# Kernel optimization log

Hardware: AMD Instinct MI355X
Metric: run time of the kernel (lower is better)

The kernel has to match this reference:

```python
import jax, jax.numpy as jnp
import numpy as np

B, P, K, KS = 512, 64, 30, 4      # graphs, nodes per graph, sort-pool k, conv1d kernel
N, E, F, H = B * P, 524288, 128, 256
N_CLASSES = 10
L_OUT = K - KS + 1                 # 27, conv1d output length


def _sage(h, wl, wr, b, src, dst, inv_deg):
    # PyG SAGEConv (mean aggr): out = lin_l(mean_j x_j) + lin_r(x_i); bias only on lin_l
    agg = jax.ops.segment_sum(h[src], dst, num_segments=N) * inv_deg
    return jax.nn.relu(agg @ wl + b + h @ wr)


def setup_inputs() -> dict:
    key = jax.random.key(0)
    ks = jax.random.split(key, 32)
    x = jax.random.normal(ks[0], (N, F), jnp.float32)
    # intra-graph random edges (src -> dst aggregation)
    g = jax.random.randint(ks[1], (E,), 0, B)
    src = g * P + jax.random.randint(ks[2], (E,), 0, P)
    dst = g * P + jax.random.randint(ks[3], (E,), 0, P)
    edge_index = jnp.stack([src, dst]).astype(jnp.int32)
    batch = jnp.repeat(jnp.arange(B), P).astype(jnp.int32)  # sorted graph ids

    def lin(k, i, o):
        return jax.random.normal(k, (i, o), jnp.float32) / np.float32(np.sqrt(i))

    inp = {"x": x, "edge_index": edge_index, "batch": batch}
    dims = [(F, H), (H, H), (H, H), (H, H)]
    ki = 4
    for li, (i, o) in enumerate(dims):
        inp[f"sage{li}_wl"] = lin(ks[ki], i, o); ki += 1
        inp[f"sage{li}_wr"] = lin(ks[ki], i, o); ki += 1
        inp[f"sage{li}_b"] = jnp.zeros((o,), jnp.float32)
    inp["conv1d_w"] = jax.random.normal(ks[ki], (H, H, KS), jnp.float32) / np.float32(np.sqrt(H * KS)); ki += 1
    inp["conv1d_b"] = jnp.zeros((H,), jnp.float32)
    inp["lin1_w"] = lin(ks[ki], H * L_OUT, H); ki += 1
    inp["lin1_b"] = jnp.zeros((H,), jnp.float32)
    inp["lin2_w"] = lin(ks[ki], H, 128); ki += 1
    inp["lin2_b"] = jnp.zeros((128,), jnp.float32)
    inp["out_w"] = lin(ks[ki], 128, N_CLASSES); ki += 1
    inp["out_b"] = jnp.zeros((N_CLASSES,), jnp.float32)
    return inp


def reference(x, edge_index, batch,
              sage0_wl, sage0_wr, sage0_b,
              sage1_wl, sage1_wr, sage1_b,
              sage2_wl, sage2_wr, sage2_b,
              sage3_wl, sage3_wr, sage3_b,
              conv1d_w, conv1d_b, lin1_w, lin1_b,
              lin2_w, lin2_b, out_w, out_b):
    src, dst = edge_index[0], edge_index[1]
    deg = jax.ops.segment_sum(jnp.ones(src.shape, x.dtype), dst, num_segments=N)
    inv_deg = (1.0 / jnp.maximum(deg, 1.0))[:, None]

    h = jnp.nan_to_num(x, nan=0.0)
    h = _sage(h, sage0_wl, sage0_wr, sage0_b, src, dst, inv_deg)
    h = _sage(h, sage1_wl, sage1_wr, sage1_b, src, dst, inv_deg)
    h = _sage(h, sage2_wl, sage2_wr, sage2_b, src, dst, inv_deg)
    h = _sage(h, sage3_wl, sage3_wr, sage3_b, src, dst, inv_deg)  # [N, H]

    # SortAggregation(k=K): to dense batch, sort by last channel desc, top-k, zero-pad
    counts = jax.ops.segment_sum(jnp.ones(N, jnp.int32), batch, num_segments=B)
    offsets = jnp.cumsum(counts) - counts
    pos = jnp.arange(N) - offsets[batch]
    D = h.shape[1]
    dense = jnp.zeros((B, P, D), h.dtype).at[batch, pos].set(h)
    valid = jnp.zeros((B, P), bool).at[batch, pos].set(True)
    skey = jnp.where(valid, dense[..., -1], -jnp.inf)
    order = jnp.argsort(-skey, axis=1)[:, :K]                       # [B, K]
    topk = jnp.take_along_axis(dense, order[..., None], axis=1)     # [B, K, D]
    tvalid = jnp.take_along_axis(valid, order, axis=1)
    topk = jnp.where(tvalid[..., None], topk, 0.0)

    # x.view(B, K, -1).permute(0, 2, 1) -> [B, D, K]
    xc = topk.transpose(0, 2, 1)
    y = jax.lax.conv_general_dilated(xc, conv1d_w, (1,), 'VALID',
                                     dimension_numbers=('NCH', 'OIH', 'NCH'))
    y = jax.nn.relu(y + conv1d_b[None, :, None])                    # [B, H, L_OUT]
    y = y.reshape(B, -1)                                            # dropout is identity in eval
    y = jax.nn.relu(y @ lin1_w + lin1_b)
    y = jax.nn.relu(y @ lin2_w + lin2_b)
    return jax.nn.relu(y @ out_w + out_b)                           # [B, N_CLASSES]
```

## Files before the change

### kernel.cpp

```cpp
#include <hip/hip_runtime.h>
#include <hip/hip_bf16.h>

#define NNODES 32768
#define NEDGES 524288
#define NGRAPH 512
#define PNODES 64
#define KTOP 30
#define FIN 128
#define HID 256
#define LOUT 27

#define C1F 4.8828125e-4f
#define C2F 2.384185791015625e-7f

using f16x8 = __attribute__((ext_vector_type(8))) _Float16;
using f16x4 = __attribute__((ext_vector_type(4))) _Float16;
using f32x4 = __attribute__((ext_vector_type(4))) float;
using f32x16 = __attribute__((ext_vector_type(16))) float;

#define GLDS(src, dst) __builtin_amdgcn_global_load_lds( \
    (const __attribute__((address_space(1))) void*)(src), \
    (__attribute__((address_space(3))) void*)(dst), 16, 0, 0)

__global__ void hist_kernel(const int* __restrict__ dst, int* __restrict__ counts) {
    int e = blockIdx.x * blockDim.x + threadIdx.x;
    if (e < NEDGES) atomicAdd(&counts[dst[e]], 1);
}

__global__ __launch_bounds__(1024) void scan_block_kernel(const int* __restrict__ counts,
        int* __restrict__ loc, int* __restrict__ partial) {
    int b = blockIdx.x, t = threadIdx.x;
    int i = b * 1024 + t;
    int v = counts[i];
    int lane = t & 63, w = t >> 6;
    int x = v;
    #pragma unroll
    for (int d = 1; d < 64; d <<= 1) { int y = __shfl_up(x, d, 64); if (lane >= d) x += y; }
    __shared__ int ws[16];
    if (lane == 63) ws[w] = x;
    __syncthreads();
    if (w == 0) {
        int s = (lane < 16) ? ws[lane] : 0;
        #pragma unroll
        for (int d = 1; d < 16; d <<= 1) { int y = __shfl_up(s, d, 64); if (lane >= d) s += y; }
        if (lane < 16) ws[lane] = s;
    }
    __syncthreads();
    int base = (w > 0) ? ws[w - 1] : 0;
    int incl = base + x;
    loc[i] = incl - v;
    if (t == 1023) partial[b] = incl;
}

__global__ __launch_bounds__(1024) void scan_fixup_kernel(const int* __restrict__ loc,
        const int* __restrict__ partial, const int* __restrict__ counts,
        int* __restrict__ offsets, int* __restrict__ cursor, float* __restrict__ invdeg) {
    int b = blockIdx.x, t = threadIdx.x;
    int i = b * 1024 + t;
    __shared__ int sbase;
    if (t == 0) { int s = 0; for (int j = 0; j < b; ++j) s += partial[j]; sbase = s; }
    __syncthreads();
    int o = loc[i] + sbase;
    offsets[i] = o;
    cursor[i] = o;
    invdeg[i] = 1.0f / fmaxf((float)counts[i], 1.0f);
}

__global__ void scatter_kernel(const int* __restrict__ src, const int* __restrict__ dst,
        int* __restrict__ cursor, int* __restrict__ ssrc) {
    int e = blockIdx.x * blockDim.x + threadIdx.x;
    if (e < NEDGES) {
        int d = dst[e];
        int p = atomicAdd(&cursor[d], 1);
        ssrc[p] = src[e];
    }
}

__global__ void nan2num_split_kernel(const float* __restrict__ x,
        _Float16* __restrict__ oh, _Float16* __restrict__ ol, int n4) {
    int i = blockIdx.x * blockDim.x + threadIdx.x;
    if (i >= n4) return;
    float4 v = *(const float4*)(x + i * 4);
    float xs[4] = {v.x, v.y, v.z, v.w};
    f16x4 hh, ll;
    #pragma unroll
    for (int q = 0; q < 4; ++q) {
        float a = xs[q];
        a = (a != a) ? 0.f : a;
        _Float16 h = (_Float16)a;
        hh[q] = h;
        ll[q] = (_Float16)((a - (float)h) * 2048.0f);
    }
    *(f16x4*)(oh + (size_t)i * 4) = hh;
    *(f16x4*)(ol + (size_t)i * 4) = ll;
}

struct Prep8 {
    const float* src[8];
    _Float16* dh[8];
    _Float16* dl[8];
    int logK[8];
    int nelem[8];
    int rstride[8];
};

__global__ __launch_bounds__(256) void prep8_kernel(Prep8 p) {
    int y = blockIdx.y;
    int idx = blockIdx.x * 256 + threadIdx.x;
    if (idx >= p.nelem[y]) return;
    int lk = p.logK[y], K = 1 << lk;
    int n = idx >> lk, k = idx & (K - 1);
    float w = p.src[y][(size_t)k * 256 + n];
    _Float16 h = (_Float16)w;
    p.dh[y][(size_t)n * p.rstride[y] + k] = h;
    p.dl[y][(size_t)n * p.rstride[y] + k] = (_Float16)((w - (float)h) * 2048.0f);
}

__global__ __launch_bounds__(256) void prep_conv_kernel(const float* __restrict__ W,
        _Float16* __restrict__ b0, _Float16* __restrict__ b1) {
    int idx = blockIdx.x * 256 + threadIdx.x;
    int o = idx >> 10, k = idx & 1023;
    float w = W[(size_t)o * 1024 + (k & 255) * 4 + (k >> 8)];
    _Float16 h = (_Float16)w;
    b0[(size_t)o * 1024 + k] = h;
    b1[(size_t)o * 1024 + k] = (_Float16)((w - (float)h) * 2048.0f);
}

__global__ __launch_bounds__(256) void prep_lin1_kernel(const float* __restrict__ l1w,
        _Float16* __restrict__ wh, _Float16* __restrict__ wl_) {
    __shared__ float sh[64][65];
    int kb = blockIdx.x * 64;
    int nb = blockIdx.y * 64;
    int t = threadIdx.x;
    {
        int kk = t >> 2;
        int nc = (t & 3) * 16;
        int k = kb + kk, l = k >> 8, c = k & 255;
        const float* srow = l1w + (size_t)(c * 27 + l) * 256 + nb + nc;
        #pragma unroll
        for (int j = 0; j < 16; j += 4) {
            float4 v = *(const float4*)(srow + j);
            sh[kk][nc + j + 0] = v.x;
            sh[kk][nc + j + 1] = v.y;
            sh[kk][nc + j + 2] = v.z;
            sh[kk][nc + j + 3] = v.w;
        }
    }
    __syncthreads();
    {
        int nn = t >> 2;
        int kc = (t & 3) * 16;
        f16x8 oh[2], ol[2];
        #pragma unroll
        for (int j = 0; j < 16; ++j) {
            float x = sh[kc + j][nn];
            _Float16 h = (_Float16)x;
            oh[j >> 3][j & 7] = h;
            ol[j >> 3][j & 7] = (_Float16)((x - (float)h) * 2048.0f);
        }
        size_t o = (size_t)(nb + nn) * 6912 + kb + kc;
        *(f16x8*)(wh + o) = oh[0];
        *(f16x8*)(wh + o + 8) = oh[1];
        *(f16x8*)(wl_ + o) = ol[0];
        *(f16x8*)(wl_ + o + 8) = ol[1];
    }
}

template<int HIN, int LOGHIN>
__global__ __launch_bounds__(512, 2) void fused_sage_kernel(
        const _Float16* __restrict__ hh, const _Float16* __restrict__ hl,
        const int* __restrict__ offsets, const int* __restrict__ counts,
        const int* __restrict__ ssrc, const float* __restrict__ invdeg,
        const _Float16* __restrict__ Wh, const _Float16* __restrict__ Wl,
        const float* __restrict__ bias,
        _Float16* __restrict__ outh, _Float16* __restrict__ outl) {
    constexpr int KV = 2 * HIN;
    constexpr int NP = HIN / 32;
    constexpr int TILE = 64 * HIN;
    __shared__ __align__(16) float hsm[TILE];
    __shared__ __align__(16) _Float16 am[2][TILE];
    _Float16* hp0 = reinterpret_cast<_Float16*>(hsm);
    _Float16* hp1 = hp0 + TILE;
    const int g = blockIdx.x, t = threadIdx.x;
    const int lane = t & 63, wave = t >> 6;
    const size_t base = (size_t)g * TILE;

    for (int i4 = t * 4; i4 < TILE; i4 += 2048) {
        f16x4 vh = *(const f16x4*)(hh + base + i4);
        f16x4 vl = *(const f16x4*)(hl + base + i4);
        int row = i4 >> LOGHIN, col = i4 & (HIN - 1);
        int sw = row & 28;
        *(float4*)&hsm[(row << LOGHIN) + (col ^ sw)] = make_float4(
            (float)vh[0] + C1F * (float)vl[0],
            (float)vh[1] + C1F * (float)vl[1],
            (float)vh[2] + C1F * (float)vl[2],
            (float)vh[3] + C1F * (float)vl[3]);
    }
    __syncthreads();

    const int node = t >> 3, q = t & 7;
    const int gnode = g * 64 + node;
    const int beg = offsets[gnode], cnt = counts[gnode];
    const float s = invdeg[gnode];
    float acc[NP][4];
    #pragma unroll
    for (int p = 0; p < NP; ++p) { acc[p][0] = 0.f; acc[p][1] = 0.f; acc[p][2] = 0.f; acc[p][3] = 0.f; }
    for (int e = 0; e < cnt; ++e) {
        int sn = ssrc[beg + e] & 63;
        int ro = sn << LOGHIN, sw = sn & 28;
        #pragma unroll
        for (int p = 0; p < NP; ++p) {
            int f = p * 32 + q * 4;
            float4 v = *(const float4*)&hsm[ro + (f ^ sw)];
            acc[p][0] += v.x; acc[p][1] += v.y; acc[p][2] += v.z; acc[p][3] += v.w;
        }
    }
    float hv[NP][4];
    {
        int ro = node << LOGHIN, sw = node & 28;
        #pragma unroll
        for (int p = 0; p < NP; ++p) {
            int f = p * 32 + q * 4;
            float4 v = *(const float4*)&hsm[ro + (f ^ sw)];
            hv[p][0] = v.x; hv[p][1] = v.y; hv[p][2] = v.z; hv[p][3] = v.w;
        }
    }
    __syncthreads();

    {
        int slot = ((q >> 1) ^ (node & 3)) * 8 + (q & 1) * 4;
        int a0 = node * 32 + slot;
        #pragma unroll
        for (int p = 0; p < NP; ++p) {
            int addr = p * 2048 + a0;
            f16x4 ah, al, bh4, bl4;
            #pragma unroll
            for (int j = 0; j < 4; ++j) {
                float va = acc[p][j] * s;
                _Float16 h1 = (_Float16)va;
                ah[j] = h1; al[j] = (_Float16)((va - (float)h1) * 2048.0f);
                float vb = hv[p][j];
                _Float16 h2 = (_Float16)vb;
                bh4[j] = h2; bl4[j] = (_Float16)((vb - (float)h2) * 2048.0f);
            }
            *(f16x4*)&am[0][addr] = ah;
            *(f16x4*)&am[1][addr] = al;
            *(f16x4*)&hp0[addr] = bh4;
            *(f16x4*)&hp1[addr] = bl4;
        }
    }
    __syncthreads();

    const int l31 = lane & 31, hb = lane >> 5;
    const int col = wave * 32 + l31;
    const _Float16* __restrict__ Brh = Wh + (size_t)col * KV;
    const _Float16* __restrict__ Brl = Wl + (size_t)col * KV;
    f32x16 acc0[2], acc1[2];
    #pragma unroll
    for (int mi = 0; mi < 2; ++mi) { acc0[mi] = 0.f; acc1[mi] = 0.f; }

    f16x8 a0f[2][2][2], a1f[2][2][2];
    f16x8 bhf[2][2], blf[2][2];
    constexpr int nC = KV / 32;

    auto loadA = [&](int c, int buf) {
        int kv = c * 32;
        const _Float16* sh = (kv < HIN) ? &am[0][0] : hp0;
        const _Float16* sl = (kv < HIN) ? &am[1][0] : hp1;
        int pbase = ((kv & (HIN - 1)) >> 5) * 2048;
        #pragma unroll
        for (int h2 = 0; h2 < 2; ++h2)
            #pragma unroll
            for (int mi = 0; mi < 2; ++mi) {
                int row = mi * 32 + l31;
                int addr = pbase + row * 32 + (((2 * h2 + hb) ^ (row & 3)) * 8);
                a0f[buf][h2][mi] = *(const f16x8*)&sh[addr];
                a1f[buf][h2][mi] = *(const f16x8*)&sl[addr];
            }
    };
    auto loadB = [&](int c, int buf) {
        int kv = c * 32;
        #pragma unroll
        for (int h2 = 0; h2 < 2; ++h2) {
            int o = kv + h2 * 16 + hb * 8;
            bhf[buf][h2] = *(const f16x8*)(Brh + o);
            blf[buf][h2] = *(const f16x8*)(Brl + o);
        }
    };

    loadA(0, 0); loadB(0, 0);
    #pragma unroll 2
    for (int c = 0; c < nC; ++c) {
        int cur = c & 1, nxt = cur ^ 1;
        if (c + 1 < nC) { loadA(c + 1, nxt); loadB(c + 1, nxt); }
        #pragma unroll
        for (int h2 = 0; h2 < 2; ++h2)
            #pragma unroll
            for (int mi = 0; mi < 2; ++mi) {
                acc0[mi] = __builtin_amdgcn_mfma_f32_32x32x16_f16(a0f[cur][h2][mi], bhf[cur][h2], acc0[mi], 0, 0, 0);
                acc1[mi] = __builtin_amdgcn_mfma_f32_32x32x16_f16(a1f[cur][h2][mi], bhf[cur][h2], acc1[mi], 0, 0, 0);
                acc1[mi] = __builtin_amdgcn_mfma_f32_32x32x16_f16(a0f[cur][h2][mi], blf[cur][h2], acc1[mi], 0, 0, 0);
            }
    }

    const int rq = 4 * hb;
    const float bb = bias[col];
    #pragma unroll
    for (int mi = 0; mi < 2; ++mi) {
        #pragma unroll
        for (int reg = 0; reg < 16; ++reg) {
            float v = acc0[mi][reg] + C1F * acc1[mi][reg];
            int row = mi * 32 + (reg & 3) + 8 * (reg >> 2) + rq;
            v = fmaxf(v + bb, 0.f);
            _Float16 h1 = (_Float16)v;
            size_t o = (size_t)(g * 64 + row) * HID + col;
            outh[o] = h1;
            outl[o] = (_Float16)((v - (float)h1) * 2048.0f);
        }
    }
}

template<int NPROD, int CONV, int NPAIRS, int EPI>
__global__ __launch_bounds__(256, 2) void mfma_ps_kernel(
        const _Float16* __restrict__ A1h, const _Float16* __restrict__ A1l,
        const _Float16* __restrict__ A2h, const _Float16* __restrict__ A2l,
        const _Float16* __restrict__ B1h, const _Float16* __restrict__ B1l,
        const _Float16* __restrict__ B2h, const _Float16* __restrict__ B2l,
        const float* __restrict__ bias,
        _Float16* __restrict__ outh, _Float16* __restrict__ outl,
        float* __restrict__ Cpart,
        int lda, int K, int Nd, int nrb) {
    __shared__ _Float16 As[2][2][128 * 32];
    __shared__ _Float16 Bs[2][2][128 * 32];
    const int t = threadIdx.x;
    const int lane = t & 63, wave = t >> 6;
    const int wr = wave & 1, wc = wave >> 1;
    const int bid = blockIdx.x;
    const int rb = bid % nrb, cb = bid / nrb;
    const int row0 = rb * 128, col0 = cb * 128;
    const int l31 = lane & 31, hb = lane >> 5, x3 = l31 & 3;
    const int r16 = lane >> 2;
    const int qsrc8 = ((lane & 3) ^ (r16 & 3)) * 8;
    size_t aoffj[2], boffj[2];
    #pragma unroll
    for (int j = 0; j < 2; ++j) {
        int ar = row0 + wave * 32 + j * 16 + r16;
        aoffj[j] = CONV ? ((size_t)ar * 256 + (size_t)(ar / 27) * 768)
                        : (size_t)ar * (size_t)lda;
        boffj[j] = (size_t)(col0 + wave * 32 + j * 16 + r16) * (size_t)K;
    }
    int aroff[2], broff[2], slot8[2];
    #pragma unroll
    for (int mi = 0; mi < 2; ++mi) aroff[mi] = (wr * 64 + mi * 32 + l31) * 32;
    #pragma unroll
    for (int ni = 0; ni < 2; ++ni) broff[ni] = (wc * 64 + ni * 32 + l31) * 32;
    #pragma unroll
    for (int h = 0; h < 2; ++h) slot8[h] = ((2 * h + hb) ^ x3) * 8;

    const int KV = NPAIRS * K;
    const int kchunk = KV / gridDim.z;
    const int kv_lo = blockIdx.z * kchunk, kv_hi = kv_lo + kchunk;

    f32x16 acc0[2][2], acc1[2][2], acc2[2][2];
    #pragma unroll
    for (int i = 0; i < 2; ++i)
        #pragma unroll
        for (int j = 0; j < 2; ++j) { acc0[i][j] = 0.f; acc1[i][j] = 0.f; acc2[i][j] = 0.f; }

    auto stage = [&](int kv, int b) {
        int p = (NPAIRS == 2 && kv >= K) ? 1 : 0;
        int k = kv - p * K;
        const _Float16* __restrict__ sAh = p ? A2h : A1h;
        const _Float16* __restrict__ sAl = p ? A2l : A1l;
        const _Float16* __restrict__ sBh = p ? B2h : B1h;
        const _Float16* __restrict__ sBl = p ? B2l : B1l;
        #pragma unroll
        for (int j = 0; j < 2; ++j) {
            int ldsbase = (wave * 32 + j * 16) * 32;
            size_t ga = aoffj[j] + k + qsrc8;
            size_t gb = boffj[j] + k + qsrc8;
            GLDS(sAh + ga, &As[b][0][ldsbase]);
            GLDS(sAl + ga, &As[b][1][ldsbase]);
            GLDS(sBh + gb, &Bs[b][0][ldsbase]);
            GLDS(sBl + gb, &Bs[b][1][ldsbase]);
        }
    };

    stage(kv_lo, 0);
    __syncthreads();
    int b = 0;
    for (int kv = kv_lo; kv < kv_hi; kv += 32) {
        if (kv + 32 < kv_hi) stage(kv + 32, b ^ 1);
        #pragma unroll
        for (int h = 0; h < 2; ++h) {
            f16x8 af0[2], af1[2], bf0[2], bf1[2];
            #pragma unroll
            for (int mi = 0; mi < 2; ++mi) {
                af0[mi] = *(const f16x8*)&As[b][0][aroff[mi] + slot8[h]];
                af1[mi] = *(const f16x8*)&As[b][1][aroff[mi] + slot8[h]];
            }
            #pragma unroll
            for (int ni = 0; ni < 2; ++ni) {
                bf0[ni] = *(const f16x8*)&Bs[b][0][broff[ni] + slot8[h]];
                bf1[ni] = *(const f16x8*)&Bs[b][1][broff[ni] + slot8[h]];
            }
            #pragma unroll
            for (int mi = 0; mi < 2; ++mi)
                #pragma unroll
                for (int ni = 0; ni < 2; ++ni) {
                    acc0[mi][ni] = __builtin_amdgcn_mfma_f32_32x32x16_f16(af0[mi], bf0[ni], acc0[mi][ni], 0, 0, 0);
                    acc1[mi][ni] = __builtin_amdgcn_mfma_f32_32x32x16_f16(af1[mi], bf0[ni], acc1[mi][ni], 0, 0, 0);
                    acc1[mi][ni] = __builtin_amdgcn_mfma_f32_32x32x16_f16(af0[mi], bf1[ni], acc1[mi][ni], 0, 0, 0);
                    if (NPROD == 4)
                        acc2[mi][ni] = __builtin_amdgcn_mfma_f32_32x32x16_f16(af1[mi], bf1[ni], acc2[mi][ni], 0, 0, 0);
                }
        }
        b ^= 1;
        __syncthreads();
    }

    const int rquad = 4 * hb;
    #pragma unroll
    for (int ni = 0; ni < 2; ++ni) {
        int col = col0 + wc * 64 + ni * 32 + l31;
        float bb = (EPI == 0) ? bias[col] : 0.f;
        #pragma unroll
        for (int mi = 0; mi < 2; ++mi) {
            #pragma unroll
            for (int reg = 0; reg < 16; ++reg) {
                float v = acc0[mi][ni][reg] + C1F * acc1[mi][ni][reg];
                if (NPROD == 4) v += C2F * acc2[mi][ni][reg];
                int row = row0 + wr * 64 + mi * 32 + (reg & 3) + 8 * (reg >> 2) + rquad;
                if (EPI == 0) {
                    v = fmaxf(v + bb, 0.f);
                    _Float16 h = (_Float16)v;
                    size_t o = (size_t)row * Nd + col;
                    outh[o] = h;
                    outl[o] = (_Float16)((v - (float)h) * 2048.0f);
                } else {
                    size_t zb = (size_t)blockIdx.z * (size_t)(nrb * 128) * Nd;
                    Cpart[zb + (size_t)row * Nd + col] = v;
                }
            }
        }
    }
}

__global__ __launch_bounds__(256) void sortgather_kernel(const _Float16* __restrict__ hh,
        const _Float16* __restrict__ hl, _Float16* __restrict__ th, _Float16* __restrict__ tl) {
    __shared__ float vals[PNODES];
    __shared__ int ord[KTOP];
    int g = blockIdx.x, t = threadIdx.x;
    if (t < PNODES) {
        size_t idx = (size_t)(g * PNODES + t) * HID + (HID - 1);
        vals[t] = (float)hh[idx] + C1F * (float)hl[idx];
    }
    __syncthreads();
    if (t < PNODES) {
        float v = vals[t];
        int rank = 0;
        for (int j = 0; j < PNODES; ++j) {
            float vj = vals[j];
            rank += (vj > v) || (vj == v && j < t);
        }
        if (rank < KTOP) ord[rank] = g * PNODES + t;
    }
    __syncthreads();
    int c8 = (t & 31) * 8;
    for (int r = t >> 5; r < KTOP; r += 8) {
        size_t s = (size_t)ord[r] * HID + c8;
        size_t d = (size_t)(g * KTOP + r) * HID + c8;
        *(f16x8*)(th + d) = *(const f16x8*)(hh + s);
        *(f16x8*)(tl + d) = *(const f16x8*)(hl + s);
    }
}

__global__ void reduce_conv_kernel(const float* __restrict__ yb32,
        const float* __restrict__ b, _Float16* __restrict__ ybh, _Float16* __restrict__ ybl) {
    int i = blockIdx.x * 256 + threadIdx.x;
    float v = fmaxf(yb32[i] + yb32[i + 13824 * 256] + b[i & 255], 0.f);
    _Float16 h = (_Float16)v;
    ybh[i] = h;
    ybl[i] = (_Float16)((v - (float)h) * 2048.0f);
}

__global__ void reduce_lin1_kernel(const float* __restrict__ z1p,
        const float* __restrict__ b, float* __restrict__ z1) {
    int i = blockIdx.x * 256 + threadIdx.x;
    float s = b[i & 255];
    #pragma unroll
    for (int z = 0; z < 27; ++z) s += z1p[(size_t)z * 131072 + i];
    z1[i] = fmaxf(s, 0.f);
}

__global__ __launch_bounds__(256) void gemm64_kernel(
        const float* __restrict__ A, const float* __restrict__ B,
        const float* __restrict__ bias, float* __restrict__ C,
        int lda, int kend, int Nd) {
    __shared__ float As[16][64];
    __shared__ float Bs[16][64];
    const int tid = threadIdx.x;
    const int tx = tid & 15, ty = tid >> 4;
    const int la_r = tid >> 2, la_c = (tid & 3) << 2;
    const int lb_r = tid >> 4, lb_c = (tid & 15) << 2;
    const int row0 = blockIdx.x * 64, col0 = blockIdx.y * 64;
    const size_t aoff = (size_t)(row0 + la_r) * (size_t)lda;
    float acc[4][4] = {};
    for (int k0 = 0; k0 < kend; k0 += 16) {
        __syncthreads();
        float4 av = *(const float4*)(A + aoff + k0 + la_c);
        As[la_c + 0][la_r] = av.x;
        As[la_c + 1][la_r] = av.y;
        As[la_c + 2][la_r] = av.z;
        As[la_c + 3][la_r] = av.w;
        *(float4*)&Bs[lb_r][lb_c] = *(const float4*)(B + (size_t)(k0 + lb_r) * Nd + col0 + lb_c);
        __syncthreads();
        #pragma unroll
        for (int k = 0; k < 16; ++k) {
            float4 a = *(const float4*)&As[k][ty << 2];
            float4 b = *(const float4*)&Bs[k][tx << 2];
            acc[0][0] += a.x * b.x; acc[0][1] += a.x * b.y; acc[0][2] += a.x * b.z; acc[0][3] += a.x * b.w;
            acc[1][0] += a.y * b.x; acc[1][1] += a.y * b.y; acc[1][2] += a.y * b.z; acc[1][3] += a.y * b.w;
            acc[2][0] += a.z * b.x; acc[2][1] += a.z * b.y; acc[2][2] += a.z * b.z; acc[2][3] += a.z * b.w;
            acc[3][0] += a.w * b.x; acc[3][1] += a.w * b.y; acc[3][2] += a.w * b.z; acc[3][3] += a.w * b.w;
        }
    }
    #pragma unroll
    for (int i = 0; i < 4; ++i) {
        int row = row0 + (ty << 2) + i;
        #pragma unroll
        for (int j = 0; j < 4; ++j) {
            int col = col0 + (tx << 2) + j;
            C[(size_t)row * Nd + col] = fmaxf(acc[i][j] + bias[col], 0.f);
        }
    }
}

__global__ void out_kernel(const float* __restrict__ z2, const float* __restrict__ w,
        const float* __restrict__ b, float* __restrict__ out) {
    int idx = blockIdx.x * blockDim.x + threadIdx.x;
    if (idx < NGRAPH * 10) {
        int r = idx / 10, c = idx % 10;
        float s = b[c];
        for (int k = 0; k < 128; ++k) s += z2[r * 128 + k] * w[k * 10 + c];
        out[idx] = fmaxf(s, 0.f);
    }
}

extern "C" void kernel_launch(void* const* d_in, const int* in_sizes, int n_in,
                              void* d_out, int out_size, void* d_ws, size_t ws_size,
                              hipStream_t stream) {
    const float* x    = (const float*)d_in[0];
    const int*   edge = (const int*)d_in[1];
    const int*   esrc = edge;
    const int*   edst = edge + NEDGES;
    const float* wl[4] = {(const float*)d_in[3], (const float*)d_in[6], (const float*)d_in[9],  (const float*)d_in[12]};
    const float* wr[4] = {(const float*)d_in[4], (const float*)d_in[7], (const float*)d_in[10], (const float*)d_in[13]};
    const float* sb[4] = {(const float*)d_in[5], (const float*)d_in[8], (const float*)d_in[11], (const float*)d_in[14]};
    const float* convw = (const float*)d_in[15];
    const float* convb = (const float*)d_in[16];
    const float* l1w   = (const float*)d_in[17];
    const float* l1b   = (const float*)d_in[18];
    const float* l2w   = (const float*)d_in[19];
    const float* l2b   = (const float*)d_in[20];
    const float* ow    = (const float*)d_in[21];
    const float* ob    = (const float*)d_in[22];
    float* out = (float*)d_out;

    char* ws = (char*)d_ws;
    size_t off = 0;
    auto alloc = [&](size_t bytes) -> char* {
        char* p = ws + off;
        off = (off + bytes + 255) & ~(size_t)255;
        return p;
    };
    int*   counts  = (int*)alloc((size_t)NNODES * 4);
    int*   offsets = (int*)alloc((size_t)NNODES * 4);
    int*   cursor  = (int*)alloc((size_t)NNODES * 4);
    int*   loc     = (int*)alloc((size_t)NNODES * 4);
    int*   partial = (int*)alloc(32 * 4);
    float* invdeg  = (float*)alloc((size_t)NNODES * 4);
    int*   ssrc    = (int*)alloc((size_t)NEDGES * 4);
    _Float16* wch[4]; _Float16* wcl[4];
    for (int l = 0; l < 4; ++l) {
        size_t kb = (size_t)256 * 2 * (l ? HID : FIN) * 2;
        wch[l] = (_Float16*)alloc(kb);
        wcl[l] = (_Float16*)alloc(kb);
    }
    _Float16* cvh = (_Float16*)alloc((size_t)HID * 1024 * 2);
    _Float16* cvl = (_Float16*)alloc((size_t)HID * 1024 * 2);

    const size_t H0T = (size_t)NNODES * FIN * 2;
    const size_t AGT = (size_t)NNODES * HID * 2;
    const size_t TKT = (size_t)NGRAPH * KTOP * HID * 2;
    const size_t YBT = (size_t)NGRAPH * LOUT * HID * 2;
    const size_t YB32T = (size_t)2 * 13824 * 256 * 4;
    const size_t Z1PT = (size_t)27 * NGRAPH * HID * 4;
    const size_t W1T = (size_t)HID * 6912 * 2;

    char* R1 = alloc(2 * H0T);
    char* R2 = alloc(2 * AGT);
    char* R3 = alloc(2 * AGT);
    char* R4 = alloc(2 * AGT);
    _Float16* h0h = (_Float16*)R1; _Float16* h0l = (_Float16*)(R1 + H0T);
    _Float16* tkh = (_Float16*)R1; _Float16* tkl = (_Float16*)(R1 + TKT);
    _Float16* hAh = (_Float16*)R3; _Float16* hAl = (_Float16*)(R3 + AGT);
    _Float16* ybh = (_Float16*)R2; _Float16* ybl_ = (_Float16*)(R2 + YBT);
    float* yb32 = (float*)(R2 + 2 * YBT);
    float* z1p  = (float*)(R2 + 2 * YBT);
    char* tail2 = R2 + 2 * YBT + YB32T;
    float* z1  = (float*)tail2;
    float* z2  = (float*)(tail2 + (size_t)NGRAPH * HID * 4);
    _Float16* w1h = (_Float16*)(tail2 + (size_t)NGRAPH * HID * 4 + (size_t)NGRAPH * 128 * 4 + 256);
    _Float16* w1l = (_Float16*)((char*)w1h + W1T);
    _Float16* hBh = (_Float16*)R4; _Float16* hBl = (_Float16*)(R4 + AGT);

    hipMemsetAsync(counts, 0, (size_t)NNODES * 4, stream);
    hist_kernel<<<NEDGES / 256, 256, 0, stream>>>(edst, counts);
    scan_block_kernel<<<NNODES / 1024, 1024, 0, stream>>>(counts, loc, partial);
    scan_fixup_kernel<<<NNODES / 1024, 1024, 0, stream>>>(loc, partial, counts, offsets, cursor, invdeg);
    scatter_kernel<<<NEDGES / 256, 256, 0, stream>>>(esrc, edst, cursor, ssrc);
    nan2num_split_kernel<<<(NNODES * FIN / 4) / 256, 256, 0, stream>>>(x, h0h, h0l, NNODES * FIN / 4);

    Prep8 p8;
    for (int l = 0; l < 4; ++l) {
        int K = l ? HID : FIN, lk = l ? 8 : 7;
        p8.src[2 * l] = wl[l];     p8.dh[2 * l] = wch[l];         p8.dl[2 * l] = wcl[l];
        p8.src[2 * l + 1] = wr[l]; p8.dh[2 * l + 1] = wch[l] + K; p8.dl[2 * l + 1] = wcl[l] + K;
        p8.logK[2 * l] = lk;     p8.nelem[2 * l] = 256 * K;     p8.rstride[2 * l] = 2 * K;
        p8.logK[2 * l + 1] = lk; p8.nelem[2 * l + 1] = 256 * K; p8.rstride[2 * l + 1] = 2 * K;
    }
    prep8_kernel<<<dim3(256, 8), 256, 0, stream>>>(p8);
    prep_conv_kernel<<<(HID * 1024) / 256, 256, 0, stream>>>(convw, cvh, cvl);

    fused_sage_kernel<FIN, 7><<<NGRAPH, 512, 0, stream>>>(
        h0h, h0l, offsets, counts, ssrc, invdeg, wch[0], wcl[0], sb[0], hAh, hAl);
    _Float16* hinh = hAh; _Float16* hinl = hAl;
    _Float16* hoth = hBh; _Float16* hotl = hBl;
    for (int l = 1; l < 4; ++l) {
        fused_sage_kernel<HID, 8><<<NGRAPH, 512, 0, stream>>>(
            hinh, hinl, offsets, counts, ssrc, invdeg, wch[l], wcl[l], sb[l], hoth, hotl);
        _Float16* t1 = hinh; hinh = hoth; hoth = t1;
        _Float16* t2 = hinl; hinl = hotl; hotl = t2;
    }

    sortgather_kernel<<<NGRAPH, 256, 0, stream>>>(hinh, hinl, tkh, tkl);
    prep_lin1_kernel<<<dim3(108, 4), 256, 0, stream>>>(l1w, w1h, w1l);

    mfma_ps_kernel<3, 1, 1, 1><<<dim3(108 * 2, 1, 2), 256, 0, stream>>>(
        tkh, tkl, nullptr, nullptr, cvh, cvl, nullptr, nullptr, nullptr, nullptr, nullptr, yb32, 256, 1024, HID, 108);
    reduce_conv_kernel<<<13824 * 256 / 256, 256, 0, stream>>>(yb32, convb, ybh, ybl_);

    mfma_ps_kernel<3, 0, 1, 1><<<dim3(4 * 2, 1, 27), 256, 0, stream>>>(
        ybh, ybl_, nullptr, nullptr, w1h, w1l, nullptr, nullptr, nullptr, nullptr, nullptr, z1p, 6912, 6912, HID, 4);
    reduce_lin1_kernel<<<NGRAPH * HID / 256, 256, 0, stream>>>(z1p, l1b, z1);

    gemm64_kernel<<<dim3(NGRAPH / 64, 128 / 64), 256, 0, stream>>>(z1, l2w, l2b, z2, HID, HID, 128);

    out_kernel<<<(NGRAPH * 10 + 255) / 256, 256, 0, stream>>>(z2, ow, ob, out);
}
```

Measured before the change: 493.8 us.

## Reformulate SAGE aggregation as dense per-graph adjacency matmul applied after projection

Rather than gathering neighbour features in fp32 LDS per edge, each block builds a 64x64 per-graph edge-count matrix in LDS via atomics, scales it by inverse degree, and computes S·(H·Wl) on MFMA after projecting H with Wl. H is staged into LDS with global_load_lds in split-fp16 form, and the weight layout is changed so Wl and Wr are stored as separate blocks. LDS use drops (launch bounds raised to 4 blocks) and the per-edge gather loop is removed, at the cost of an extra small GEMM and rounding the intermediate H·Wl into split fp16.

```diff
diff --git a/kernel.cpp b/kernel.cpp
--- a/kernel.cpp
+++ b/kernel.cpp
@@ -72,7 +72,7 @@
     if (e < NEDGES) {
         int d = dst[e];
         int p = atomicAdd(&cursor[d], 1);
-        ssrc[p] = src[e];
+        ssrc[p] = ((d & 63) << 6) | (src[e] & 63);
     }
 }
 
@@ -166,154 +166,171 @@
     }
 }
 
-template<int HIN, int LOGHIN>
-__global__ __launch_bounds__(512, 2) void fused_sage_kernel(
+template<int HIN>
+__global__ __launch_bounds__(512, 4) void fused_sage2_kernel(
         const _Float16* __restrict__ hh, const _Float16* __restrict__ hl,
         const int* __restrict__ offsets, const int* __restrict__ counts,
         const int* __restrict__ ssrc, const float* __restrict__ invdeg,
-        const _Float16* __restrict__ Wh, const _Float16* __restrict__ Wl,
+        const _Float16* __restrict__ Wh, const _Float16* __restrict__ Wl_,
         const float* __restrict__ bias,
         _Float16* __restrict__ outh, _Float16* __restrict__ outl) {
-    constexpr int KV = 2 * HIN;
-    constexpr int NP = HIN / 32;
-    constexpr int TILE = 64 * HIN;
-    __shared__ __align__(16) float hsm[TILE];
-    __shared__ __align__(16) _Float16 am[2][TILE];
-    _Float16* hp0 = reinterpret_cast<_Float16*>(hsm);
-    _Float16* hp1 = hp0 + TILE;
+    constexpr int NCH = HIN / 32;
+    __shared__ __align__(16) _Float16 hp[2][NCH * 2048];
+    __shared__ __align__(16) uint32_t Sw[4096];
     const int g = blockIdx.x, t = threadIdx.x;
     const int lane = t & 63, wave = t >> 6;
-    const size_t base = (size_t)g * TILE;
-
-    for (int i4 = t * 4; i4 < TILE; i4 += 2048) {
-        f16x4 vh = *(const f16x4*)(hh + base + i4);
-        f16x4 vl = *(const f16x4*)(hl + base + i4);
-        int row = i4 >> LOGHIN, col = i4 & (HIN - 1);
-        int sw = row & 28;
-        *(float4*)&hsm[(row << LOGHIN) + (col ^ sw)] = make_float4(
-            (float)vh[0] + C1F * (float)vl[0],
-            (float)vh[1] + C1F * (float)vl[1],
-            (float)vh[2] + C1F * (float)vl[2],
-            (float)vh[3] + C1F * (float)vl[3]);
-    }
-    __syncthreads();
-
-    const int node = t >> 3, q = t & 7;
-    const int gnode = g * 64 + node;
-    const int beg = offsets[gnode], cnt = counts[gnode];
-    const float s = invdeg[gnode];
-    float acc[NP][4];
-    #pragma unroll
-    for (int p = 0; p < NP; ++p) { acc[p][0] = 0.f; acc[p][1] = 0.f; acc[p][2] = 0.f; acc[p][3] = 0.f; }
-    for (int e = 0; e < cnt; ++e) {
-        int sn = ssrc[beg + e] & 63;
-        int ro = sn << LOGHIN, sw = sn & 28;
-        #pragma unroll
-        for (int p = 0; p < NP; ++p) {
-            int f = p * 32 + q * 4;
-            float4 v = *(const float4*)&hsm[ro + (f ^ sw)];
-            acc[p][0] += v.x; acc[p][1] += v.y; acc[p][2] += v.z; acc[p][3] += v.w;
-        }
-    }
-    float hv[NP][4];
+    const int l31 = lane & 31, hb = lane >> 5;
+    const size_t gbase = (size_t)g * 64 * HIN;
+
+    #pragma unroll
+    for (int i = 0; i < 8; ++i) Sw[t + i * 512] = 0;
+
     {
-        int ro = node << LOGHIN, sw = node & 28;
-        #pragma unroll
-        for (int p = 0; p < NP; ++p) {
-            int f = p * 32 + q * 4;
-            float4 v = *(const float4*)&hsm[ro + (f ^ sw)];
-            hv[p][0] = v.x; hv[p][1] = v.y; hv[p][2] = v.z; hv[p][3] = v.w;
-        }
-    }
+        int a = lane >> 2, b = lane & 3;
+        for (int u = wave; u < NCH * 8; u += 8) {
+            int part = u & 1;
+            int cs = u >> 1;
+            int c = cs >> 2, stripe = cs & 3;
+            int row = stripe * 16 + a;
+            int o = b ^ ((row >> 1) & 3) ^ (c & 3);
+            const _Float16* src = (part ? hl : hh) + gbase + (size_t)row * HIN + c * 32 + o * 8;
+            GLDS(src, &hp[part][c * 2048 + stripe * 512]);
+        }
+    }
+
+    const int gbeg = offsets[g * 64];
+    const int gend = offsets[g * 64 + 63] + counts[g * 64 + 63];
+    __syncthreads();
+
+    for (int e = gbeg + t; e < gend; e += 512)
+        atomicAdd(&Sw[ssrc[e] & 4095], 1u);
     __syncthreads();
 
     {
-        int slot = ((q >> 1) ^ (node & 3)) * 8 + (q & 1) * 4;
-        int a0 = node * 32 + slot;
-        #pragma unroll
-        for (int p = 0; p < NP; ++p) {
-            int addr = p * 2048 + a0;
-            f16x4 ah, al, bh4, bl4;
+        int d = t >> 3, o = t & 7;
+        float idg = invdeg[g * 64 + d];
+        float v[8];
+        #pragma unroll
+        for (int j = 0; j < 8; ++j) v[j] = (float)Sw[(d << 6) + (o << 3) + j] * idg;
+        __syncthreads();
+        _Float16* Sp = (_Float16*)Sw;
+        f16x8 s0, s1;
+        #pragma unroll
+        for (int j = 0; j < 8; ++j) {
+            _Float16 h1 = (_Float16)v[j];
+            s0[j] = h1;
+            s1[j] = (_Float16)((v[j] - (float)h1) * 2048.0f);
+        }
+        int addr = (d << 6) + ((o ^ (d & 7)) << 3);
+        *(f16x8*)&Sp[addr] = s0;
+        *(f16x8*)&Sp[4096 + addr] = s1;
+    }
+    __syncthreads();
+
+    const int col = (wave << 5) + l31;
+
+    auto gemmKV = [&](const _Float16* __restrict__ Bh, const _Float16* __restrict__ Bl,
+                      f32x16* a0, f32x16* a1) {
+        #pragma unroll 2
+        for (int c = 0; c < NCH; ++c) {
+            #pragma unroll
+            for (int h2 = 0; h2 < 2; ++h2) {
+                f16x8 ah[2], al_[2];
+                #pragma unroll
+                for (int mi = 0; mi < 2; ++mi) {
+                    int row = (mi << 5) + l31;
+                    int slot = (2 * h2 + hb) ^ ((row >> 1) & 3) ^ (c & 3);
+                    int addr = c * 2048 + (row << 5) + (slot << 3);
+                    ah[mi] = *(const f16x8*)&hp[0][addr];
+                    al_[mi] = *(const f16x8*)&hp[1][addr];
+                }
+                int ko = (c << 5) + (h2 << 4) + (hb << 3);
+                f16x8 bh = *(const f16x8*)(Bh + ko);
+                f16x8 bl = *(const f16x8*)(Bl + ko);
+                #pragma unroll
+                for (int mi = 0; mi < 2; ++mi) {
+                    a0[mi] = __builtin_amdgcn_mfma_f32_32x32x16_f16(ah[mi], bh, a0[mi], 0, 0, 0);
+                    a1[mi] = __builtin_amdgcn_mfma_f32_32x32x16_f16(al_[mi], bh, a1[mi], 0, 0, 0);
+                    a1[mi] = __builtin_amdgcn_mfma_f32_32x32x16_f16(ah[mi], bl, a1[mi], 0, 0, 0);
+                }
+            }
+        }
+    };
+
+    f32x16 acc0[2], acc1[2];
+    acc0[0] = 0.f; acc0[1] = 0.f; acc1[0] = 0.f; acc1[1] = 0.f;
+    gemmKV(Wh + (size_t)col * HIN, Wl_ + (size_t)col * HIN, acc0, acc1);
+    f32x16 pf[2];
+    pf[0] = acc0[0] + C1F * acc1[0];
+    pf[1] = acc0[1] + C1F * acc1[1];
+
+    f32x16 so0[2], so1[2];
+    so0[0] = 0.f; so0[1] = 0.f; so1[0] = 0.f; so1[1] = 0.f;
+    {
+        const _Float16* Sp = (const _Float16*)Sw;
+        #pragma unroll
+        for (int kc = 0; kc < 4; ++kc) {
+            float kv[4], sv[4];
             #pragma unroll
             for (int j = 0; j < 4; ++j) {
-                float va = acc[p][j] * s;
-                _Float16 h1 = (_Float16)va;
-                ah[j] = h1; al[j] = (_Float16)((va - (float)h1) * 2048.0f);
-                float vb = hv[p][j];
-                _Float16 h2 = (_Float16)vb;
-                bh4[j] = h2; bl4[j] = (_Float16)((vb - (float)h2) * 2048.0f);
+                float e0 = pf[(2 * kc) >> 2][((2 * kc) & 3) * 4 + j];
+                float e1 = pf[(2 * kc + 1) >> 2][((2 * kc + 1) & 3) * 4 + j];
+                kv[j] = hb ? e1 : e0;
+                sv[j] = hb ? e0 : e1;
             }
-            *(f16x4*)&am[0][addr] = ah;
-            *(f16x4*)&am[1][addr] = al;
-            *(f16x4*)&hp0[addr] = bh4;
-            *(f16x4*)&hp1[addr] = bl4;
-        }
-    }
-    __syncthreads();
-
-    const int l31 = lane & 31, hb = lane >> 5;
-    const int col = wave * 32 + l31;
-    const _Float16* __restrict__ Brh = Wh + (size_t)col * KV;
-    const _Float16* __restrict__ Brl = Wl + (size_t)col * KV;
-    f32x16 acc0[2], acc1[2];
-    #pragma unroll
-    for (int mi = 0; mi < 2; ++mi) { acc0[mi] = 0.f; acc1[mi] = 0.f; }
-
-    f16x8 a0f[2][2][2], a1f[2][2][2];
-    f16x8 bhf[2][2], blf[2][2];
-    constexpr int nC = KV / 32;
-
-    auto loadA = [&](int c, int buf) {
-        int kv = c * 32;
-        const _Float16* sh = (kv < HIN) ? &am[0][0] : hp0;
-        const _Float16* sl = (kv < HIN) ? &am[1][0] : hp1;
-        int pbase = ((kv & (HIN - 1)) >> 5) * 2048;
-        #pragma unroll
-        for (int h2 = 0; h2 < 2; ++h2)
+            uint32_t kh[2], kl2[2], sh_[2], sl2[2];
+            #pragma unroll
+            for (int q = 0; q < 2; ++q) {
+                union { uint32_t u; _Float16 f[2]; } H1, L1, H2, L2;
+                #pragma unroll
+                for (int j = 0; j < 2; ++j) {
+                    float x = kv[q * 2 + j];
+                    _Float16 h1 = (_Float16)x;
+                    H1.f[j] = h1; L1.f[j] = (_Float16)((x - (float)h1) * 2048.0f);
+                    float y = sv[q * 2 + j];
+                    _Float16 h2 = (_Float16)y;
+                    H2.f[j] = h2; L2.f[j] = (_Float16)((y - (float)h2) * 2048.0f);
+                }
+                kh[q] = H1.u; kl2[q] = L1.u; sh_[q] = H2.u; sl2[q] = L2.u;
+            }
+            uint32_t rh0 = (uint32_t)__shfl_xor((int)sh_[0], 32, 64);
+            uint32_t rh1 = (uint32_t)__shfl_xor((int)sh_[1], 32, 64);
+            uint32_t rl0 = (uint32_t)__shfl_xor((int)sl2[0], 32, 64);
+            uint32_t rl1 = (uint32_t)__shfl_xor((int)sl2[1], 32, 64);
+            union { uint32_t u[4]; f16x8 v; } bh_, bl_;
+            bh_.u[0] = hb ? rh0 : kh[0];  bh_.u[1] = hb ? rh1 : kh[1];
+            bh_.u[2] = hb ? kh[0] : rh0;  bh_.u[3] = hb ? kh[1] : rh1;
+            bl_.u[0] = hb ? rl0 : kl2[0]; bl_.u[1] = hb ? rl1 : kl2[1];
+            bl_.u[2] = hb ? kl2[0] : rl0; bl_.u[3] = hb ? kl2[1] : rl1;
             #pragma unroll
             for (int mi = 0; mi < 2; ++mi) {
-                int row = mi * 32 + l31;
-                int addr = pbase + row * 32 + (((2 * h2 + hb) ^ (row & 3)) * 8);
-                a0f[buf][h2][mi] = *(const f16x8*)&sh[addr];
-                a1f[buf][h2][mi] = *(const f16x8*)&sl[addr];
+                int row = (mi << 5) + l31;
+                int soff = (row << 6) + (((2 * kc + hb) ^ (row & 7)) << 3);
+                f16x8 s0f = *(const f16x8*)&Sp[soff];
+                f16x8 s1f = *(const f16x8*)&Sp[4096 + soff];
+                so0[mi] = __builtin_amdgcn_mfma_f32_32x32x16_f16(s0f, bh_.v, so0[mi], 0, 0, 0);
+                so1[mi] = __builtin_amdgcn_mfma_f32_32x32x16_f16(s0f, bl_.v, so1[mi], 0, 0, 0);
+                so1[mi] = __builtin_amdgcn_mfma_f32_32x32x16_f16(s1f, bh_.v, so1[mi], 0, 0, 0);
             }
-    };
-    auto loadB = [&](int c, int buf) {
-        int kv = c * 32;
-        #pragma unroll
-        for (int h2 = 0; h2 < 2; ++h2) {
-            int o = kv + h2 * 16 + hb * 8;
-            bhf[buf][h2] = *(const f16x8*)(Brh + o);
-            blf[buf][h2] = *(const f16x8*)(Brl + o);
-        }
-    };
-
-    loadA(0, 0); loadB(0, 0);
-    #pragma unroll 2
-    for (int c = 0; c < nC; ++c) {
-        int cur = c & 1, nxt = cur ^ 1;
-        if (c + 1 < nC) { loadA(c + 1, nxt); loadB(c + 1, nxt); }
-        #pragma unroll
-        for (int h2 = 0; h2 < 2; ++h2)
-            #pragma unroll
-            for (int mi = 0; mi < 2; ++mi) {
-                acc0[mi] = __builtin_amdgcn_mfma_f32_32x32x16_f16(a0f[cur][h2][mi], bhf[cur][h2], acc0[mi], 0, 0, 0);
-                acc1[mi] = __builtin_amdgcn_mfma_f32_32x32x16_f16(a1f[cur][h2][mi], bhf[cur][h2], acc1[mi], 0, 0, 0);
-                acc1[mi] = __builtin_amdgcn_mfma_f32_32x32x16_f16(a0f[cur][h2][mi], blf[cur][h2], acc1[mi], 0, 0, 0);
-            }
-    }
-
-    const int rq = 4 * hb;
+        }
+    }
+    f32x16 sC[2];
+    sC[0] = so0[0] + C1F * so1[0];
+    sC[1] = so0[1] + C1F * so1[1];
+
+    acc0[0] = 0.f; acc0[1] = 0.f; acc1[0] = 0.f; acc1[1] = 0.f;
+    gemmKV(Wh + (size_t)(256 + col) * HIN, Wl_ + (size_t)(256 + col) * HIN, acc0, acc1);
+
     const float bb = bias[col];
     #pragma unroll
     for (int mi = 0; mi < 2; ++mi) {
         #pragma unroll
         for (int reg = 0; reg < 16; ++reg) {
-            float v = acc0[mi][reg] + C1F * acc1[mi][reg];
-            int row = mi * 32 + (reg & 3) + 8 * (reg >> 2) + rq;
-            v = fmaxf(v + bb, 0.f);
+            float v = sC[mi][reg] + acc0[mi][reg] + C1F * acc1[mi][reg] + bb;
+            v = fmaxf(v, 0.f);
+            int row = (mi << 5) + (reg & 3) + ((reg >> 2) << 3) + (hb << 2);
             _Float16 h1 = (_Float16)v;
-            size_t o = (size_t)(g * 64 + row) * HID + col;
+            size_t o = (size_t)((g << 6) + row) * HID + col;
             outh[o] = h1;
             outl[o] = (_Float16)((v - (float)h1) * 2048.0f);
         }
@@ -583,7 +600,7 @@
     int*   ssrc    = (int*)alloc((size_t)NEDGES * 4);
     _Float16* wch[4]; _Float16* wcl[4];
     for (int l = 0; l < 4; ++l) {
-        size_t kb = (size_t)256 * 2 * (l ? HID : FIN) * 2;
+        size_t kb = (size_t)512 * (l ? HID : FIN) * 2;
         wch[l] = (_Float16*)alloc(kb);
         wcl[l] = (_Float16*)alloc(kb);
     }
@@ -595,7 +612,6 @@
     const size_t TKT = (size_t)NGRAPH * KTOP * HID * 2;
     const size_t YBT = (size_t)NGRAPH * LOUT * HID * 2;
     const size_t YB32T = (size_t)2 * 13824 * 256 * 4;
-    const size_t Z1PT = (size_t)27 * NGRAPH * HID * 4;
     const size_t W1T = (size_t)HID * 6912 * 2;
 
     char* R1 = alloc(2 * H0T);
@@ -625,20 +641,20 @@
     Prep8 p8;
     for (int l = 0; l < 4; ++l) {
         int K = l ? HID : FIN, lk = l ? 8 : 7;
-        p8.src[2 * l] = wl[l];     p8.dh[2 * l] = wch[l];         p8.dl[2 * l] = wcl[l];
-        p8.src[2 * l + 1] = wr[l]; p8.dh[2 * l + 1] = wch[l] + K; p8.dl[2 * l + 1] = wcl[l] + K;
-        p8.logK[2 * l] = lk;     p8.nelem[2 * l] = 256 * K;     p8.rstride[2 * l] = 2 * K;
-        p8.logK[2 * l + 1] = lk; p8.nelem[2 * l + 1] = 256 * K; p8.rstride[2 * l + 1] = 2 * K;
+        p8.src[2 * l] = wl[l];     p8.dh[2 * l] = wch[l];                 p8.dl[2 * l] = wcl[l];
+        p8.src[2 * l + 1] = wr[l]; p8.dh[2 * l + 1] = wch[l] + 256 * K;  p8.dl[2 * l + 1] = wcl[l] + 256 * K;
+        p8.logK[2 * l] = lk;     p8.nelem[2 * l] = 256 * K;     p8.rstride[2 * l] = K;
+        p8.logK[2 * l + 1] = lk; p8.nelem[2 * l + 1] = 256 * K; p8.rstride[2 * l + 1] = K;
     }
     prep8_kernel<<<dim3(256, 8), 256, 0, stream>>>(p8);
     prep_conv_kernel<<<(HID * 1024) / 256, 256, 0, stream>>>(convw, cvh, cvl);
 
-    fused_sage_kernel<FIN, 7><<<NGRAPH, 512, 0, stream>>>(
+    fused_sage2_kernel<FIN><<<NGRAPH, 512, 0, stream>>>(
         h0h, h0l, offsets, counts, ssrc, invdeg, wch[0], wcl[0], sb[0], hAh, hAl);
     _Float16* hinh = hAh; _Float16* hinl = hAl;
     _Float16* hoth = hBh; _Float16* hotl = hBl;
     for (int l = 1; l < 4; ++l) {
-        fused_sage_kernel<HID, 8><<<NGRAPH, 512, 0, stream>>>(
+        fused_sage2_kernel<HID><<<NGRAPH, 512, 0, stream>>>(
             hinh, hinl, offsets, counts, ssrc, invdeg, wch[l], wcl[l], sb[l], hoth, hotl);
         _Float16* t1 = hinh; hinh = hoth; hoth = t1;
         _Float16* t2 = hinl; hinl = hotl; hotl = t2;
```

Result: faster. 481.1 us (-2.6%).
